# Kernel tuning notes

Hardware: AMD Instinct MI355X
Metric: run time of the kernel (lower is better)

Reference implementation:

```python
import jax, jax.numpy as jnp
import numpy as np

B, IN_DIM, OUT_DIM = 262144, 2, 256


def setup_inputs() -> dict:
    key = jax.random.key(0)
    k1, k2, k3 = jax.random.split(key, 3)
    x = jax.random.normal(k1, (B, IN_DIM), dtype=jnp.float32)
    h = jax.random.normal(k2, (OUT_DIM, IN_DIM), dtype=jnp.float32) * 0.01
    delta = jax.random.normal(k3, (OUT_DIM,), dtype=jnp.float32) * 0.01
    return {"x": x, "h": h, "delta": delta}


def reference(x, h, delta):
    # z = F.linear(x, h): [B, OUT_DIM]
    theta = x @ h.T + delta  # phase argument, delta broadcast over batch
    out_real = jnp.cos(theta)
    out_imag = jnp.sin(theta)
    # S_proxy = diag_embed(mean_b out_complex); eigvals of a diagonal matrix
    # are its diagonal entries, so angles are arctan2(mean_imag, mean_real).
    mean_r = out_real.mean(axis=0)  # [OUT_DIM]
    mean_i = out_imag.mean(axis=0)  # [OUT_DIM]
    eta = jnp.sum(jnp.arctan2(mean_i, mean_r)) / jnp.pi
    return out_real, eta
```

## Files before the change

kernel.cpp:

```cpp
#include <hip/hip_runtime.h>
#include <math.h>


#define B_DIM 262144
#define O_DIM 256
#define NB1 2048
#define NB2 64
#define ROWS_PER_BLOCK (B_DIM / NB1)
#define ROWS_PER_WAVE (ROWS_PER_BLOCK / 4)

typedef float vf4 __attribute__((ext_vector_type(4)));

__global__ __launch_bounds__(256) void fdc_main(
    const float* __restrict__ x, const float* __restrict__ h,
    const float* __restrict__ delta, float* __restrict__ out,
    float* __restrict__ partial ) {
  const int tid  = threadIdx.x;
  const int lane = tid & 63;
  const int wv   = tid >> 6;
  const int col4 = lane * 4;

  const float4* h4 = (const float4*)h;
  const float4 ha = h4[lane * 2];
  const float4 hb = h4[lane * 2 + 1];
  const float4 dl = ((const float4*)delta)[lane];

  __shared__ float2 xs[ROWS_PER_BLOCK];
  ((float*)xs)[tid] = x[(size_t)blockIdx.x * (ROWS_PER_BLOCK * 2) + tid];
  __syncthreads();

  vf4* out4 = (vf4*)out;
  float sc0 = 0.f, sc1 = 0.f, sc2 = 0.f, sc3 = 0.f;
  float ss0 = 0.f, ss1 = 0.f, ss2 = 0.f, ss3 = 0.f;

  const int rbase = blockIdx.x * ROWS_PER_BLOCK + wv * ROWS_PER_WAVE;
  const int lbase = wv * ROWS_PER_WAVE;
#pragma unroll 4
  for (int i = 0; i < ROWS_PER_WAVE; ++i) {
    const float2 xv = xs[lbase + i];
    const int row = rbase + i;
    float s, c;
    vf4 o;
    const float t0 = fmaf(xv.x, ha.x, fmaf(xv.y, ha.y, dl.x));
    const float t1 = fmaf(xv.x, ha.z, fmaf(xv.y, ha.w, dl.y));
    const float t2 = fmaf(xv.x, hb.x, fmaf(xv.y, hb.y, dl.z));
    const float t3 = fmaf(xv.x, hb.z, fmaf(xv.y, hb.w, dl.w));
    __sincosf(t0, &s, &c); o.x = c; sc0 += c; ss0 += s;
    __sincosf(t1, &s, &c); o.y = c; sc1 += c; ss1 += s;
    __sincosf(t2, &s, &c); o.z = c; sc2 += c; ss2 += s;
    __sincosf(t3, &s, &c); o.w = c; sc3 += c; ss3 += s;
    __builtin_nontemporal_store(o, &out4[(size_t)row * 64 + lane]);
  }

  __shared__ float lds[4][512];
  lds[wv][col4 + 0] = sc0; lds[wv][col4 + 1] = sc1;
  lds[wv][col4 + 2] = sc2; lds[wv][col4 + 3] = sc3;
  lds[wv][256 + col4 + 0] = ss0; lds[wv][256 + col4 + 1] = ss1;
  lds[wv][256 + col4 + 2] = ss2; lds[wv][256 + col4 + 3] = ss3;
  __syncthreads();
  const float a = lds[0][tid] + lds[1][tid] + lds[2][tid] + lds[3][tid];
  const float b = lds[0][tid + 256] + lds[1][tid + 256] +
                  lds[2][tid + 256] + lds[3][tid + 256];
  float* p = partial + (size_t)blockIdx.x * 512;
  p[tid] = a;
  p[256 + tid] = b;
}

__global__ __launch_bounds__(256) void fdc_red1(
    const float* __restrict__ partial, float* __restrict__ partial2) {
  const int t = threadIdx.x;
  const float* base = partial + (size_t)blockIdx.x * (NB1 / NB2) * 512;
  float cs = 0.f, sn = 0.f;
#pragma unroll 8
  for (int r = 0; r < NB1 / NB2; ++r) {
    cs += base[r * 512 + t];
    sn += base[r * 512 + 256 + t];
  }
  partial2[(size_t)blockIdx.x * 512 + t] = cs;
  partial2[(size_t)blockIdx.x * 512 + 256 + t] = sn;
}

__global__ __launch_bounds__(256) void fdc_red2(
    const float* __restrict__ partial2, float* __restrict__ out) {
  const int t = threadIdx.x;
  float cs = 0.f, sn = 0.f;
#pragma unroll 4
  for (int r = 0; r < NB2; ++r) {
    cs += partial2[(size_t)r * 512 + t];
    sn += partial2[(size_t)r * 512 + 256 + t];
  }
  float ang = atan2f(sn, cs);
  __shared__ float red[256];
  red[t] = ang;
  __syncthreads();
  for (int st = 128; st > 0; st >>= 1) {
    if (t < st) red[t] += red[t + st];
    __syncthreads();
  }
  if (t == 0) out[(size_t)B_DIM * O_DIM] = red[0] * (float)(1.0 / M_PI);
}

extern "C" void kernel_launch(void* const* d_in, const int* in_sizes, int n_in,
                              void* d_out, int out_size, void* d_ws, size_t ws_size,
                              hipStream_t stream) {
  const float* x     = (const float*)d_in[0];
  const float* h     = (const float*)d_in[1];
  const float* delta = (const float*)d_in[2];
  float* out = (float*)d_out;
  float* partial  = (float*)d_ws;
  float* partial2 = partial + (size_t)NB1 * 512;
  (void)ws_size;

  fdc_main<<<NB1, 256, 0, stream>>>(x, h, delta, out, partial);
  fdc_red1<<<NB2, 256, 0, stream>>>(partial, partial2);
  fdc_red2<<<1, 256, 0, stream>>>(partial2, out);
}
```

Before: 276.4 us.

## Replace two-stage partial reduction with slotted atomic accumulation

Each main block now atomically adds its per-column cos/sin sums into one of 8 accumulator slots instead of writing a partial row. This removes the intermediate reduction kernel and its partial-buffer traffic, at the cost of adding a small zero-init kernel and contended float atomics, which also make the summation order nondeterministic. The final kernel reduces only 8 slots.

Result: faster. 270.5 us (-2.1%).

```diff
diff --git a/kernel.cpp b/kernel.cpp
--- a/kernel.cpp
+++ b/kernel.cpp
@@ -5,16 +5,20 @@
 #define B_DIM 262144
 #define O_DIM 256
 #define NB1 2048
-#define NB2 64
 #define ROWS_PER_BLOCK (B_DIM / NB1)
 #define ROWS_PER_WAVE (ROWS_PER_BLOCK / 4)
+#define NSLOT 8
 
 typedef float vf4 __attribute__((ext_vector_type(4)));
+
+__global__ __launch_bounds__(256) void fdc_init(float* __restrict__ acc) {
+  acc[(size_t)blockIdx.x * 256 + threadIdx.x] = 0.f;
+}
 
 __global__ __launch_bounds__(256) void fdc_main(
     const float* __restrict__ x, const float* __restrict__ h,
     const float* __restrict__ delta, float* __restrict__ out,
-    float* __restrict__ partial ) {
+    float* __restrict__ acc ) {
   const int tid  = threadIdx.x;
   const int lane = tid & 63;
   const int wv   = tid >> 6;
@@ -61,33 +65,20 @@
   const float a = lds[0][tid] + lds[1][tid] + lds[2][tid] + lds[3][tid];
   const float b = lds[0][tid + 256] + lds[1][tid + 256] +
                   lds[2][tid + 256] + lds[3][tid + 256];
-  float* p = partial + (size_t)blockIdx.x * 512;
-  p[tid] = a;
-  p[256 + tid] = b;
+
+  float* slot = acc + (size_t)(blockIdx.x & (NSLOT - 1)) * 512;
+  atomicAdd(slot + tid, a);
+  atomicAdd(slot + 256 + tid, b);
 }
 
-__global__ __launch_bounds__(256) void fdc_red1(
-    const float* __restrict__ partial, float* __restrict__ partial2) {
-  const int t = threadIdx.x;
-  const float* base = partial + (size_t)blockIdx.x * (NB1 / NB2) * 512;
-  float cs = 0.f, sn = 0.f;
-#pragma unroll 8
-  for (int r = 0; r < NB1 / NB2; ++r) {
-    cs += base[r * 512 + t];
-    sn += base[r * 512 + 256 + t];
-  }
-  partial2[(size_t)blockIdx.x * 512 + t] = cs;
-  partial2[(size_t)blockIdx.x * 512 + 256 + t] = sn;
-}
-
-__global__ __launch_bounds__(256) void fdc_red2(
-    const float* __restrict__ partial2, float* __restrict__ out) {
+__global__ __launch_bounds__(256) void fdc_fin(
+    const float* __restrict__ acc, float* __restrict__ out) {
   const int t = threadIdx.x;
   float cs = 0.f, sn = 0.f;
-#pragma unroll 4
-  for (int r = 0; r < NB2; ++r) {
-    cs += partial2[(size_t)r * 512 + t];
-    sn += partial2[(size_t)r * 512 + 256 + t];
+#pragma unroll
+  for (int r = 0; r < NSLOT; ++r) {
+    cs += acc[(size_t)r * 512 + t];
+    sn += acc[(size_t)r * 512 + 256 + t];
   }
   float ang = atan2f(sn, cs);
   __shared__ float red[256];
@@ -107,11 +98,10 @@
   const float* h     = (const float*)d_in[1];
   const float* delta = (const float*)d_in[2];
   float* out = (float*)d_out;
-  float* partial  = (float*)d_ws;
-  float* partial2 = partial + (size_t)NB1 * 512;
+  float* acc = (float*)d_ws;
   (void)ws_size;
 
-  fdc_main<<<NB1, 256, 0, stream>>>(x, h, delta, out, partial);
-  fdc_red1<<<NB2, 256, 0, stream>>>(partial, partial2);
-  fdc_red2<<<1, 256, 0, stream>>>(partial2, out);
+  fdc_init<<<NSLOT * 2, 256, 0, stream>>>(acc);
+  fdc_main<<<NB1, 256, 0, stream>>>(x, h, delta, out, acc);
+  fdc_fin<<<1, 256, 0, stream>>>(acc, out);
 }
```
